# Performance work log

Hardware: AMD Instinct MI355X
Metric: run time of the kernel (lower is better)

## Reference

```python
import jax, jax.numpy as jnp
import numpy as np

EPS = 1e-07
B, H, W_IN = 128, 32, 32
N_CAPS, K_SEC, D_SEC, P_PRIM = 4608, 2, 16, 32


def setup_inputs() -> dict:
    key = jax.random.key(0)
    ks = jax.random.split(key, 12)
    input_x = jax.random.normal(ks[0], (B, H, W_IN, 1), dtype=jnp.float32)
    labels = jax.random.randint(ks[1], (B,), 0, K_SEC)
    y = jax.nn.one_hot(labels, K_SEC, dtype=jnp.float32)
    s = 0.05
    conv1_w = jax.random.normal(ks[2], (9, 9, 1, 256), dtype=jnp.float32) * s
    conv1_b = jnp.zeros((256,), dtype=jnp.float32)
    conv2_w = jax.random.normal(ks[3], (9, 9, 256, 1024), dtype=jnp.float32) * s
    conv2_b = jnp.zeros((1024,), dtype=jnp.float32)
    w = jax.random.normal(ks[4], (1, N_CAPS, K_SEC, D_SEC, P_PRIM), dtype=jnp.float32) * s
    d1_w = jax.random.normal(ks[5], (K_SEC * D_SEC, 256), dtype=jnp.float32) * s
    d1_b = jnp.zeros((256,), dtype=jnp.float32)
    d2_w = jax.random.normal(ks[6], (256, 512), dtype=jnp.float32) * s
    d2_b = jnp.zeros((512,), dtype=jnp.float32)
    d3_w = jax.random.normal(ks[7], (512, 1024), dtype=jnp.float32) * s
    d3_b = jnp.zeros((1024,), dtype=jnp.float32)
    return {"input_x": input_x, "y": y, "conv1_w": conv1_w, "conv1_b": conv1_b,
            "conv2_w": conv2_w, "conv2_b": conv2_b, "w": w,
            "d1_w": d1_w, "d1_b": d1_b, "d2_w": d2_w, "d2_b": d2_b,
            "d3_w": d3_w, "d3_b": d3_b}


def _conv(x, k, b, strides, padding):
    y = jax.lax.conv_general_dilated(x, k, strides, padding,
                                     dimension_numbers=("NHWC", "HWIO", "NHWC"))
    return y + b


def _squash(s):
    # s: [..., D]; squash along last axis
    s_norm = jnp.linalg.norm(s, axis=-1, keepdims=True)
    return (jnp.square(s_norm) / (1.0 + jnp.square(s_norm))) * s / (s_norm + EPS)


def reference(input_x, y, conv1_w, conv1_b, conv2_w, conv2_b, w,
              d1_w, d1_b, d2_w, d2_b, d3_w, d3_b):
    # Conv stack: [B,32,32,1] -> relu conv 9x9 valid -> [B,24,24,256]
    x = jax.nn.relu(_conv(input_x, conv1_w, conv1_b, (1, 1), "VALID"))
    # primary capsule conv 9x9 stride 2 'same': -> [B,12,12,1024]
    x = _conv(x, conv2_w, conv2_b, (2, 2), "SAME")

    # Capsule formation: [B,12,12,1024] -> u [B,4608,32]
    u = x.reshape(x.shape[0], N_CAPS, P_PRIM)
    # u_hat[b,n,k,d] = sum_p w[0,n,k,d,p] * u[b,n,p]
    u_hat = jnp.einsum("nkdp,bnp->bnkd", w[0], u)  # [B,4608,K,D]

    # Dynamic routing (r iterations)
    b_logits = jnp.zeros(u_hat.shape[:3] + (1,), dtype=u_hat.dtype)  # [B,N,K,1]
    v = None
    for _ in range(3):
        c = jax.nn.softmax(b_logits, axis=-2)               # softmax over K
        s = jnp.sum(c * u_hat, axis=1, keepdims=True)       # [B,1,K,D]
        v = _squash(s)                                      # [B,1,K,D]
        agreement = jnp.sum(u_hat * v, axis=-1, keepdims=True)  # [B,N,K,1]
        b_logits = b_logits + agreement

    # Masking with one-hot labels
    mask = y[:, None, :, None]                              # [B,1,K,1]
    v_masked = mask * v                                     # [B,1,K,D]

    # Reconstruction MLP (dropouts in source are no-ops)
    v_flat = v_masked.reshape(-1, K_SEC * D_SEC)            # [B,32]
    h1 = jax.nn.relu(v_flat @ d1_w + d1_b)
    h2 = jax.nn.relu(h1 @ d2_w + d2_b)
    recon = jax.nn.sigmoid(h2 @ d3_w + d3_b)                # [B,1024]
    return v, recon
```

## Files before the change

### kernel.cpp

```cpp
#include <hip/hip_runtime.h>
#include <hip/hip_bf16.h>

typedef __attribute__((ext_vector_type(8))) short s16x8;
typedef __attribute__((ext_vector_type(4))) int   i32x4;
typedef __attribute__((ext_vector_type(4))) float f32x4;

#define NCAPS 4608
#define BATCH 128

#define GLOAD_LDS16(gp, lp)                                                   \
  __builtin_amdgcn_global_load_lds(                                           \
      (const __attribute__((address_space(1))) void*)(gp),                    \
      (__attribute__((address_space(3))) void*)(lp), 16, 0, 0)

__device__ __forceinline__ float bf2f(short h) {
  union { unsigned u; float f; } cv;
  cv.u = ((unsigned)(unsigned short)h) << 16;
  return cv.f;
}

__global__ void transpose_w_kernel(const float* __restrict__ W,
                                   __hip_bfloat16* __restrict__ Wt) {
  __shared__ float tile[64][65];
  int kt = blockIdx.x * 64;
  int ct = blockIdx.y * 64;
  for (int i = threadIdx.x; i < 64 * 64; i += 256) {
    int r = i >> 6, c = i & 63;
    tile[r][c] = W[(size_t)(kt + r) * 1024 + ct + c];
  }
  __syncthreads();
  for (int i = threadIdx.x; i < 64 * 64; i += 256) {
    int r = i >> 6, c = i & 63;
    Wt[(size_t)(ct + r) * 20736 + kt + c] = __float2bfloat16(tile[c][r]);
  }
}

__global__ void conv1_kernel(const float* __restrict__ x,
                             const float* __restrict__ w,
                             const float* __restrict__ bias,
                             __hip_bfloat16* __restrict__ outp) {
  int by = blockIdx.x;
  int b = by / 24, y = by % 24;
  __shared__ float patch[288];
  for (int i = threadIdx.x; i < 288; i += 256) {
    int r = i >> 5, c = i & 31;
    patch[i] = x[(size_t)b * 1024 + (y + r) * 32 + c];
  }
  __syncthreads();
  int co = threadIdx.x;
  float bv = bias[co];
  float acc[24];
#pragma unroll
  for (int i = 0; i < 24; i++) acc[i] = bv;
#pragma unroll
  for (int ky = 0; ky < 9; ky++) {
    float row[32];
#pragma unroll
    for (int c = 0; c < 32; c++) row[c] = patch[ky * 32 + c];
#pragma unroll
    for (int kx = 0; kx < 9; kx++) {
      float wv = w[(ky * 9 + kx) * 256 + co];
#pragma unroll
      for (int xx = 0; xx < 24; xx++) acc[xx] += row[kx + xx] * wv;
    }
  }
  size_t obase = (((size_t)b * 31 + (y + 3)) * 31 + 3) * 256 + co;
#pragma unroll
  for (int xx = 0; xx < 24; xx++)
    outp[obase + (size_t)xx * 256] = __float2bfloat16(fmaxf(acc[xx], 0.f));
}

__global__ __launch_bounds__(256)
void conv2_mfma_kernel(const __hip_bfloat16* __restrict__ Apad,
                       const __hip_bfloat16* __restrict__ Wt,
                       const float* __restrict__ bias,
                       float* __restrict__ U) {
  __shared__ __align__(16) __hip_bfloat16 As[128 * 64];
  __shared__ __align__(16) __hip_bfloat16 Bs[128 * 64];
  int l = blockIdx.x;
  int s = l >> 7;
  int w0 = l & 127;
  int xcd = w0 & 7;
  int j = w0 >> 3;
  int bm = s * 16 + xcd * 2 + (j & 1);
  int bn = j >> 1;

  int tid = threadIdx.x;
  int lane = tid & 63, w = tid >> 6;
  int seg  = lane & 7;
  int rsub = lane >> 3;
  int sseg = seg ^ rsub;

  const __hip_bfloat16* abase[4];
  const __hip_bfloat16* bbase[4];
#pragma unroll
  for (int i = 0; i < 4; i++) {
    int r = w * 32 + i * 8 + rsub;
    int m = bm * 128 + r;
    int b = m / 144, rem = m % 144;
    int oy = rem / 12, ox = rem % 12;
    abase[i] = Apad + (((size_t)(b * 31 + oy * 2)) * 31 + ox * 2) * 256 + sseg * 8;
    int n = bn * 128 + r;
    bbase[i] = Wt + (size_t)n * 20736 + sseg * 8;
  }

  f32x4 acc[4][4];
#pragma unroll
  for (int mi = 0; mi < 4; mi++)
#pragma unroll
    for (int ni = 0; ni < 4; ni++)
#pragma unroll
      for (int r = 0; r < 4; r++) acc[mi][ni][r] = 0.f;

  int wm = w >> 1, wn = w & 1;
  int lrow = lane & 15;
  int lq = lane >> 4;

  for (int pos = 0; pos < 81; pos++) {
    int ky = pos / 9, kx = pos % 9;
    size_t aoff = (size_t)(ky * 31 + kx) * 256;
    size_t boff = (size_t)pos * 256;
#pragma unroll
    for (int ci0 = 0; ci0 < 256; ci0 += 64) {
#pragma unroll
      for (int i = 0; i < 4; i++) {
        GLOAD_LDS16(abase[i] + aoff + ci0, &As[(w * 32 + i * 8) * 64]);
        GLOAD_LDS16(bbase[i] + boff + ci0, &Bs[(w * 32 + i * 8) * 64]);
      }
      __syncthreads();
#pragma unroll
      for (int ksub = 0; ksub < 2; ksub++) {
        s16x8 af[4], bf[4];
#pragma unroll
        for (int mi = 0; mi < 4; mi++) {
          int row = wm * 64 + mi * 16 + lrow;
          int c = (ksub * 4 + lq) ^ (row & 7);
          af[mi] = *(const s16x8*)(As + row * 64 + c * 8);
        }
#pragma unroll
        for (int ni = 0; ni < 4; ni++) {
          int row = wn * 64 + ni * 16 + lrow;
          int c = (ksub * 4 + lq) ^ (row & 7);
          bf[ni] = *(const s16x8*)(Bs + row * 64 + c * 8);
        }
#pragma unroll
        for (int mi = 0; mi < 4; mi++)
#pragma unroll
          for (int ni = 0; ni < 4; ni++)
            acc[mi][ni] = __builtin_amdgcn_mfma_f32_16x16x32_bf16(
                af[mi], bf[ni], acc[mi][ni], 0, 0, 0);
      }
      __syncthreads();
    }
  }

#pragma unroll
  for (int mi = 0; mi < 4; mi++) {
    int mg = bm * 128 + wm * 64 + mi * 16 + ((lane >> 4) << 2);
#pragma unroll
    for (int ni = 0; ni < 4; ni++) {
      int ng = bn * 128 + wn * 64 + ni * 16 + (lane & 15);
      float bv = bias[ng];
#pragma unroll
      for (int r = 0; r < 4; r++)
        U[(size_t)(mg + r) * 1024 + ng] = acc[mi][ni][r] + bv;
    }
  }
}

__global__ void uhat_kernel(const float* __restrict__ u,
                            const float* __restrict__ w,
                            __hip_bfloat16* __restrict__ uhat) {
  int n = blockIdx.x;
  __shared__ float wsm[32 * 33];
  int t = threadIdx.x;
  for (int i = t; i < 1024; i += 256)
    wsm[(i >> 5) * 33 + (i & 31)] = w[(size_t)n * 1024 + i];
  __syncthreads();
  int kd = t & 31, bs = t >> 5;
  float wr[32];
#pragma unroll
  for (int p = 0; p < 32; p++) wr[p] = wsm[kd * 33 + p];
  for (int bp = 0; bp < 16; bp++) {
    int b = bp * 8 + bs;
    size_t off = ((size_t)b * NCAPS + n) * 32 + kd;
    float uval = u[off];
    float acc = 0.f;
#pragma unroll
    for (int p = 0; p < 32; p++) acc += wr[p] * __shfl(uval, p, 32);
    uhat[off] = __float2bfloat16(acc);
  }
}

__global__ __launch_bounds__(512)
void routing_decoder_kernel(const __hip_bfloat16* __restrict__ uhat,
                            const float* __restrict__ y,
                            const float* __restrict__ d1_w,
                            const float* __restrict__ d1_b,
                            const float* __restrict__ d2_w,
                            const float* __restrict__ d2_b,
                            const float* __restrict__ d3_w,
                            const float* __restrict__ d3_b,
                            float* __restrict__ out) {
  int b = blockIdx.x;
  int t = threadIdx.x;
  int lane = t & 63, wid = t >> 6;
  __shared__ float vls[32];
  __shared__ float red[8][32];
  __shared__ float vms[32];
  __shared__ float h1s[256];
  __shared__ float h2s[512];
  float a1c0[9], a1c1[9];
  const __hip_bfloat16* ub = uhat + (size_t)b * NCAPS * 32;

  for (int it = 0; it < 3; ++it) {
    float part[32];
#pragma unroll
    for (int d = 0; d < 32; ++d) part[d] = 0.f;
    float v0[16], v1[16];
    if (it > 0) {
#pragma unroll
      for (int d = 0; d < 16; ++d) { v0[d] = vls[d]; v1[d] = vls[16 + d]; }
    }
#pragma unroll
    for (int i = 0; i < 9; ++i) {
      int n = t + 512 * i;
      const s16x8* up8 = (const s16x8*)(ub + (size_t)n * 32);
      float uh[32];
#pragma unroll
      for (int q = 0; q < 4; ++q) {
        s16x8 raw = up8[q];
#pragma unroll
        for (int jj = 0; jj < 8; ++jj) uh[q * 8 + jj] = bf2f(raw[jj]);
      }
      float c0 = 0.5f, c1 = 0.5f;
      if (it > 0) {
        float d0 = 0.f, d1 = 0.f;
#pragma unroll
        for (int d = 0; d < 16; ++d) { d0 += uh[d] * v0[d]; d1 += uh[16 + d] * v1[d]; }
        float b0, b1;
        if (it == 1) { a1c0[i] = d0; a1c1[i] = d1; b0 = d0; b1 = d1; }
        else         { b0 = a1c0[i] + d0; b1 = a1c1[i] + d1; }
        float mx = fmaxf(b0, b1);
        float e0 = __expf(b0 - mx), e1 = __expf(b1 - mx);
        float inv = 1.f / (e0 + e1);
        c0 = e0 * inv; c1 = e1 * inv;
      }
#pragma unroll
      for (int d = 0; d < 16; ++d) {
        part[d]      += c0 * uh[d];
        part[16 + d] += c1 * uh[16 + d];
      }
    }
#pragma unroll
    for (int m = 1; m < 64; m <<= 1)
#pragma unroll
      for (int d = 0; d < 32; ++d) part[d] += __shfl_xor(part[d], m, 64);
    __syncthreads();
    if (lane == 0)
#pragma unroll
      for (int d = 0; d < 32; ++d) red[wid][d] = part[d];
    __syncthreads();
    if (t < 32) {
      float sd = 0.f;
#pragma unroll
      for (int w2 = 0; w2 < 8; ++w2) sd += red[w2][t];
      float p = sd * sd;
#pragma unroll
      for (int m = 1; m < 16; m <<= 1) p += __shfl_xor(p, m, 64);
      float f = p / (1.f + p) / (sqrtf(p) + 1e-7f);
      vls[t] = sd * f;
    }
    __syncthreads();
  }

  if (t < 32) {
    float vv = vls[t];
    out[(size_t)b * 32 + t] = vv;
    vms[t] = y[b * 2 + (t >> 4)] * vv;
  }
  __syncthreads();
  if (t < 256) {
    float acc = d1_b[t];
#pragma unroll
    for (int k = 0; k < 32; ++k) acc += vms[k] * d1_w[k * 256 + t];
    h1s[t] = fmaxf(acc, 0.f);
  }
  __syncthreads();
  {
    float acc = d2_b[t];
    for (int k = 0; k < 256; ++k) acc += h1s[k] * d2_w[k * 512 + t];
    h2s[t] = fmaxf(acc, 0.f);
  }
  __syncthreads();
  float* rout = out + 4096 + (size_t)b * 1024;
#pragma unroll
  for (int jj = 0; jj < 2; ++jj) {
    int jcol = t + jj * 512;
    float acc = d3_b[jcol];
    for (int k = 0; k < 512; ++k) acc += h2s[k] * d3_w[k * 1024 + jcol];
    rout[jcol] = 1.f / (1.f + __expf(-acc));
  }
}

extern "C" void kernel_launch(void* const* d_in, const int* in_sizes, int n_in,
                              void* d_out, int out_size, void* d_ws, size_t ws_size,
                              hipStream_t stream) {
  const float* input_x = (const float*)d_in[0];
  const float* y       = (const float*)d_in[1];
  const float* conv1_w = (const float*)d_in[2];
  const float* conv1_b = (const float*)d_in[3];
  const float* conv2_w = (const float*)d_in[4];
  const float* conv2_b = (const float*)d_in[5];
  const float* w_caps  = (const float*)d_in[6];
  const float* d1_w    = (const float*)d_in[7];
  const float* d1_b    = (const float*)d_in[8];
  const float* d2_w    = (const float*)d_in[9];
  const float* d2_b    = (const float*)d_in[10];
  const float* d3_w    = (const float*)d_in[11];
  const float* d3_b    = (const float*)d_in[12];
  float* out = (float*)d_out;

  char* ws = (char*)d_ws;
  size_t apad_bytes = (size_t)128 * 31 * 31 * 256 * 2;
  __hip_bfloat16* Apad = (__hip_bfloat16*)ws; ws += (apad_bytes + 255) & ~255ull;
  __hip_bfloat16* Wt   = (__hip_bfloat16*)ws; ws += 42467328;
  float* u             = (float*)ws;          ws += 75497472;
  __hip_bfloat16* uhat = (__hip_bfloat16*)ws; ws += 37748736;

  hipMemsetAsync(Apad, 0, apad_bytes, stream);
  transpose_w_kernel<<<dim3(324, 16), 256, 0, stream>>>(conv2_w, Wt);
  conv1_kernel<<<3072, 256, 0, stream>>>(input_x, conv1_w, conv1_b, Apad);
  conv2_mfma_kernel<<<1152, 256, 0, stream>>>(Apad, Wt, conv2_b, u);
  uhat_kernel<<<NCAPS, 256, 0, stream>>>(u, w_caps, uhat);
  routing_decoder_kernel<<<128, 512, 0, stream>>>(uhat, y, d1_w, d1_b, d2_w,
                                                  d2_b, d3_w, d3_b, out);
}
```

Before: 1.377 ms.

## Merge weight transpose with conv1 and store conv2 output in bf16

The conv2 weight transpose and conv1 are combined into one kernel that picks its job from the block index, which removes one launch and lets the two independent jobs run side by side. The conv2 output u is now written as bf16 instead of fp32, halving its write traffic and the uhat kernel's read traffic. The cost is lower precision on the intermediate capsule inputs before the u_hat projection.

```diff
diff --git a/kernel.cpp b/kernel.cpp
--- a/kernel.cpp
+++ b/kernel.cpp
@@ -19,62 +19,64 @@
   return cv.f;
 }
 
-__global__ void transpose_w_kernel(const float* __restrict__ W,
-                                   __hip_bfloat16* __restrict__ Wt) {
-  __shared__ float tile[64][65];
-  int kt = blockIdx.x * 64;
-  int ct = blockIdx.y * 64;
-  for (int i = threadIdx.x; i < 64 * 64; i += 256) {
-    int r = i >> 6, c = i & 63;
-    tile[r][c] = W[(size_t)(kt + r) * 1024 + ct + c];
-  }
-  __syncthreads();
-  for (int i = threadIdx.x; i < 64 * 64; i += 256) {
-    int r = i >> 6, c = i & 63;
-    Wt[(size_t)(ct + r) * 20736 + kt + c] = __float2bfloat16(tile[c][r]);
-  }
-}
-
-__global__ void conv1_kernel(const float* __restrict__ x,
-                             const float* __restrict__ w,
-                             const float* __restrict__ bias,
-                             __hip_bfloat16* __restrict__ outp) {
-  int by = blockIdx.x;
-  int b = by / 24, y = by % 24;
-  __shared__ float patch[288];
-  for (int i = threadIdx.x; i < 288; i += 256) {
-    int r = i >> 5, c = i & 31;
-    patch[i] = x[(size_t)b * 1024 + (y + r) * 32 + c];
-  }
-  __syncthreads();
-  int co = threadIdx.x;
-  float bv = bias[co];
-  float acc[24];
-#pragma unroll
-  for (int i = 0; i < 24; i++) acc[i] = bv;
-#pragma unroll
-  for (int ky = 0; ky < 9; ky++) {
-    float row[32];
-#pragma unroll
-    for (int c = 0; c < 32; c++) row[c] = patch[ky * 32 + c];
-#pragma unroll
-    for (int kx = 0; kx < 9; kx++) {
-      float wv = w[(ky * 9 + kx) * 256 + co];
-#pragma unroll
-      for (int xx = 0; xx < 24; xx++) acc[xx] += row[kx + xx] * wv;
-    }
-  }
-  size_t obase = (((size_t)b * 31 + (y + 3)) * 31 + 3) * 256 + co;
-#pragma unroll
-  for (int xx = 0; xx < 24; xx++)
-    outp[obase + (size_t)xx * 256] = __float2bfloat16(fmaxf(acc[xx], 0.f));
+__global__ void prep_kernel(const float* __restrict__ W,
+                            __hip_bfloat16* __restrict__ Wt,
+                            const float* __restrict__ x,
+                            const float* __restrict__ w1,
+                            const float* __restrict__ bias1,
+                            __hip_bfloat16* __restrict__ Apad) {
+  __shared__ float smem[64 * 65];
+  int bid = blockIdx.x;
+  if (bid < 5184) {
+    int kt = (bid % 324) * 64;
+    int ct = (bid / 324) * 64;
+    for (int i = threadIdx.x; i < 64 * 64; i += 256) {
+      int r = i >> 6, c = i & 63;
+      smem[r * 65 + c] = W[(size_t)(kt + r) * 1024 + ct + c];
+    }
+    __syncthreads();
+    for (int i = threadIdx.x; i < 64 * 64; i += 256) {
+      int r = i >> 6, c = i & 63;
+      Wt[(size_t)(ct + r) * 20736 + kt + c] = __float2bfloat16(smem[c * 65 + r]);
+    }
+  } else {
+    int by = bid - 5184;
+    int b = by / 24, y = by % 24;
+    float* patch = smem;
+    for (int i = threadIdx.x; i < 288; i += 256) {
+      int r = i >> 5, c = i & 31;
+      patch[i] = x[(size_t)b * 1024 + (y + r) * 32 + c];
+    }
+    __syncthreads();
+    int co = threadIdx.x;
+    float bv = bias1[co];
+    float acc[24];
+#pragma unroll
+    for (int i = 0; i < 24; i++) acc[i] = bv;
+#pragma unroll
+    for (int ky = 0; ky < 9; ky++) {
+      float row[32];
+#pragma unroll
+      for (int c = 0; c < 32; c++) row[c] = patch[ky * 32 + c];
+#pragma unroll
+      for (int kx = 0; kx < 9; kx++) {
+        float wv = w1[(ky * 9 + kx) * 256 + co];
+#pragma unroll
+        for (int xx = 0; xx < 24; xx++) acc[xx] += row[kx + xx] * wv;
+      }
+    }
+    size_t obase = (((size_t)b * 31 + (y + 3)) * 31 + 3) * 256 + co;
+#pragma unroll
+    for (int xx = 0; xx < 24; xx++)
+      Apad[obase + (size_t)xx * 256] = __float2bfloat16(fmaxf(acc[xx], 0.f));
+  }
 }
 
 __global__ __launch_bounds__(256)
 void conv2_mfma_kernel(const __hip_bfloat16* __restrict__ Apad,
                        const __hip_bfloat16* __restrict__ Wt,
                        const float* __restrict__ bias,
-                       float* __restrict__ U) {
+                       __hip_bfloat16* __restrict__ U) {
   __shared__ __align__(16) __hip_bfloat16 As[128 * 64];
   __shared__ __align__(16) __hip_bfloat16 Bs[128 * 64];
   int l = blockIdx.x;
@@ -163,12 +165,12 @@
       float bv = bias[ng];
 #pragma unroll
       for (int r = 0; r < 4; r++)
-        U[(size_t)(mg + r) * 1024 + ng] = acc[mi][ni][r] + bv;
-    }
-  }
-}
-
-__global__ void uhat_kernel(const float* __restrict__ u,
+        U[(size_t)(mg + r) * 1024 + ng] = __float2bfloat16(acc[mi][ni][r] + bv);
+    }
+  }
+}
+
+__global__ void uhat_kernel(const __hip_bfloat16* __restrict__ u,
                             const float* __restrict__ w,
                             __hip_bfloat16* __restrict__ uhat) {
   int n = blockIdx.x;
@@ -184,7 +186,7 @@
   for (int bp = 0; bp < 16; bp++) {
     int b = bp * 8 + bs;
     size_t off = ((size_t)b * NCAPS + n) * 32 + kd;
-    float uval = u[off];
+    float uval = bf2f(*(const short*)(u + off));
     float acc = 0.f;
 #pragma unroll
     for (int p = 0; p < 32; p++) acc += wr[p] * __shfl(uval, p, 32);
@@ -325,12 +327,12 @@
   size_t apad_bytes = (size_t)128 * 31 * 31 * 256 * 2;
   __hip_bfloat16* Apad = (__hip_bfloat16*)ws; ws += (apad_bytes + 255) & ~255ull;
   __hip_bfloat16* Wt   = (__hip_bfloat16*)ws; ws += 42467328;
-  float* u             = (float*)ws;          ws += 75497472;
+  __hip_bfloat16* u    = (__hip_bfloat16*)ws; ws += 37748736;
   __hip_bfloat16* uhat = (__hip_bfloat16*)ws; ws += 37748736;
 
   hipMemsetAsync(Apad, 0, apad_bytes, stream);
-  transpose_w_kernel<<<dim3(324, 16), 256, 0, stream>>>(conv2_w, Wt);
-  conv1_kernel<<<3072, 256, 0, stream>>>(input_x, conv1_w, conv1_b, Apad);
+  prep_kernel<<<8256, 256, 0, stream>>>(conv2_w, Wt, input_x, conv1_w,
+                                        conv1_b, Apad);
   conv2_mfma_kernel<<<1152, 256, 0, stream>>>(Apad, Wt, conv2_b, u);
   uhat_kernel<<<NCAPS, 256, 0, stream>>>(u, w_caps, uhat);
   routing_decoder_kernel<<<128, 512, 0, stream>>>(uhat, y, d1_w, d1_b, d2_w,
```

Result: no change. 1.351 ms (median of 2 runs) (-1.9%).
